# Kernel tuning notes

Hardware: AMD Instinct MI355X
Metric: run time of the kernel (lower is better)

## Reference

```python
import jax, jax.numpy as jnp
import numpy as np
from jax import lax

FEAT_STRIDE = 16
NMS_THRESH = 0.7
N_PRE = 6000   # test-mode n_test_pre_nms
N_POST = 300   # test-mode n_test_post_nms
MIN_SIZE = 16.0
SCALE = 1.0
RATIOS = (0.5, 1.0, 2.0)
ANCHOR_SCALES = (8, 16, 32)
BASE = 16
N_ANCHOR = len(RATIOS) * len(ANCHOR_SCALES)  # 9


def _anchor_base():
    py = px = BASE / 2.0
    ab = np.zeros((N_ANCHOR, 4), np.float32)
    for i, r in enumerate(RATIOS):
        for j, s in enumerate(ANCHOR_SCALES):
            h = BASE * s * np.sqrt(r)
            w = BASE * s * np.sqrt(1.0 / r)
            k = i * len(ANCHOR_SCALES) + j
            ab[k] = [py - h / 2.0, px - w / 2.0, py + h / 2.0, px + w / 2.0]
    return ab


def _anchors(hh, ww):
    # enumerate_shifted_anchor: (y1,x1,y2,x2) anchors for every feature cell
    ab = _anchor_base()
    sy = np.arange(0, hh * FEAT_STRIDE, FEAT_STRIDE)
    sx = np.arange(0, ww * FEAT_STRIDE, FEAT_STRIDE)
    SX, SY = np.meshgrid(sx, sy)
    shift = np.stack([SY.ravel(), SX.ravel(), SY.ravel(), SX.ravel()], 1)
    anc = (ab[None, :, :] + shift[:, None, :]).reshape(-1, 4).astype(np.float32)
    return jnp.asarray(anc)


def _iou(b):
    # b: [N,4] (y1,x1,y2,x2) -> [N,N] IoU
    y1, x1, y2, x2 = b[:, 0], b[:, 1], b[:, 2], b[:, 3]
    area = (y2 - y1) * (x2 - x1)
    ih = jnp.clip(jnp.minimum(y2[:, None], y2[None, :]) - jnp.maximum(y1[:, None], y1[None, :]), 0.0)
    iw = jnp.clip(jnp.minimum(x2[:, None], x2[None, :]) - jnp.maximum(x1[:, None], x1[None, :]), 0.0)
    inter = ih * iw
    return inter / (area[:, None] + area[None, :] - inter + 1e-9)


def _propose(loc, fg, anchor, img_h, img_w):
    # loc:[M,4] fg:[M] anchor:[M,4]  -> padded [N_POST,4] rois + valid mask
    ah = anchor[:, 2] - anchor[:, 0]
    aw = anchor[:, 3] - anchor[:, 1]
    acy = anchor[:, 0] + 0.5 * ah
    acx = anchor[:, 1] + 0.5 * aw
    cy = loc[:, 0] * ah + acy
    cx = loc[:, 1] * aw + acx
    h = jnp.exp(loc[:, 2]) * ah
    w = jnp.exp(loc[:, 3]) * aw
    roi = jnp.stack([
        jnp.clip(cy - 0.5 * h, 0.0, img_h),
        jnp.clip(cx - 0.5 * w, 0.0, img_w),
        jnp.clip(cy + 0.5 * h, 0.0, img_h),
        jnp.clip(cx + 0.5 * w, 0.0, img_w),
    ], axis=1)
    hs = roi[:, 2] - roi[:, 0]
    ws = roi[:, 3] - roi[:, 1]
    ms = MIN_SIZE * SCALE
    valid = (hs >= ms) & (ws >= ms)
    sc = jnp.where(valid, fg, -jnp.inf)  # drop too-small boxes from ranking
    top_sc, idx = lax.top_k(sc, N_PRE)   # score-sorted pre-NMS candidates
    boxes = roi[idx]
    ok = lax.stop_gradient(jnp.isfinite(top_sc))
    sup = lax.stop_gradient(_iou(boxes) > NMS_THRESH)  # [N_PRE,N_PRE]
    tri = jnp.arange(N_PRE)

    def body(i, keep):
        suppressed = jnp.any(keep & sup[:, i] & (tri < i))
        return keep.at[i].set(ok[i] & ~suppressed)

    keep = lax.fori_loop(0, N_PRE, body, jnp.zeros((N_PRE,), bool))
    rank = jnp.cumsum(keep.astype(jnp.int32)) - 1
    sel = keep & (rank < N_POST)
    tgt = jnp.where(sel, rank, N_POST)  # N_POST is out-of-bounds -> dropped
    out = jnp.zeros((N_POST, 4), boxes.dtype).at[tgt].set(boxes, mode='drop')
    vmask = jnp.zeros((N_POST,), bool).at[tgt].set(True, mode='drop')
    return out, vmask


def reference(x, conv1_w, conv1_b, score_w, score_b, loc_w, loc_b, img_h, img_w):
    n, _, hh, ww = x.shape
    anchor = _anchors(hh, ww)
    h = jax.nn.relu(
        lax.conv_general_dilated(x, conv1_w, (1, 1), 'SAME',
                                 dimension_numbers=('NCHW', 'OIHW', 'NCHW'))
        + conv1_b[None, :, None, None])
    locs = jnp.einsum('nchw,oc->nohw', h, loc_w[:, :, 0, 0]) + loc_b[None, :, None, None]
    scr = jnp.einsum('nchw,oc->nohw', h, score_w[:, :, 0, 0]) + score_b[None, :, None, None]
    rpn_locs = locs.transpose(0, 2, 3, 1).reshape(n, -1, 4)          # [n,M,4]
    scr_t = scr.transpose(0, 2, 3, 1)                                 # [n,hh,ww,2A]
    soft = jax.nn.softmax(scr_t.reshape(n, hh, ww, N_ANCHOR, 2), axis=-1)
    fg = soft[..., 1].reshape(n, -1)                                  # [n,M]
    rpn_scores = scr_t.reshape(n, -1, 2)
    rois, vmask = jax.vmap(lambda l, f: _propose(l, f, anchor, img_h, img_w))(rpn_locs, fg)
    roi_indices = jnp.broadcast_to(jnp.arange(n, dtype=jnp.int32)[:, None], (n, N_POST))
    return rpn_locs, rpn_scores, rois, roi_indices, anchor, vmask


def setup_inputs() -> dict:
    key = jax.random.key(0)
    ks = jax.random.split(key, 4)
    x = jax.random.normal(ks[0], (2, 512, 64, 64), jnp.float32)
    conv1_w = 0.01 * jax.random.normal(ks[1], (512, 512, 3, 3), jnp.float32)
    conv1_b = jnp.zeros((512,), jnp.float32)
    score_w = 0.01 * jax.random.normal(ks[2], (N_ANCHOR * 2, 512, 1, 1), jnp.float32)
    score_b = jnp.zeros((N_ANCHOR * 2,), jnp.float32)
    loc_w = 0.01 * jax.random.normal(ks[3], (N_ANCHOR * 4, 512, 1, 1), jnp.float32)
    loc_b = jnp.zeros((N_ANCHOR * 4,), jnp.float32)
    return {"x": x, "conv1_w": conv1_w, "conv1_b": conv1_b,
            "score_w": score_w, "score_b": score_b,
            "loc_w": loc_w, "loc_b": loc_b,
            "img_h": 1024, "img_w": 1024}
```

## Files before the change

### kernel.cpp

```cpp
#include <hip/hip_runtime.h>
#include <hip/hip_bf16.h>
#include <math.h>
#include <cstdint>

typedef unsigned long long u64;
typedef unsigned int u32;
typedef _Float16 half8 __attribute__((ext_vector_type(8)));
typedef float floatx4 __attribute__((ext_vector_type(4)));

#define NANCH 36864
#define SEG 65536
#define N_PRE 6000
#define N_POST 300
#define NW 96
#define NPADC 6144
#define CAP 8192

#define O0 0
#define O1 294912
#define O2 442368
#define O3 444768
#define O4 445368
#define O5 592824

#define WS_XHI   0
#define WS_XLO   2097152
#define WS_WHI   4194304
#define WS_WLO   5373952
#define WS_WSLT  6553600
#define WS_WSLB  6586368
#define WS_H     6586432
#define WS_GUARD 10780736
#define WS_FG    0
#define WS_ROI   73728
#define WS_KEYS  368640
#define WS_SBOX  630784
#define WS_ALIVE 679936
#define WS_CBUF  680320
#define WS_HIST  713088
#define WS_CNT   844160
#define WS_MASK  4194304

#define HSCALE 9.5367431640625e-07f

__device__ __forceinline__ void gl_lds16(const void* g, void* l) {
  __builtin_amdgcn_global_load_lds(
      (const __attribute__((address_space(1))) u32*)g,
      (__attribute__((address_space(3))) u32*)l, 16, 0, 0);
}

__device__ __forceinline__ u64 bcast64(u64 v, int src) {
  u32 lo = (u32)__shfl((int)(v & 0xFFFFFFFFull), src);
  u32 hi = (u32)__shfl((int)(v >> 32), src);
  return ((u64)hi << 32) | lo;
}

__global__ __launch_bounds__(256) void prep_all(
    const float* __restrict__ x, const float* __restrict__ w,
    const float* __restrict__ lw, const float* __restrict__ sw,
    const float* __restrict__ lb, const float* __restrict__ sb,
    float4* __restrict__ h, float4* __restrict__ guard,
    _Float16* __restrict__ xhi, _Float16* __restrict__ xlo,
    _Float16* __restrict__ whi, _Float16* __restrict__ wlo,
    float* __restrict__ wslt, float* __restrict__ wslb) {
  __shared__ float s[64 * 65];
  const int b = blockIdx.x, tid = threadIdx.x;
  if (b < 4097) {
    int idx = b * 256 + tid;
    if (idx < 1048576) h[idx] = make_float4(0.f, 0.f, 0.f, 0.f);
    else if (idx < 1048576 + 16) guard[idx - 1048576] = make_float4(0.f, 0.f, 0.f, 0.f);
    return;
  }
  if (b < 5121) {
    int l = b - 4097;
    int pt = l & 63, cg = (l >> 6) & 7, n = l >> 9;
    const int c0 = cg << 6, p0 = pt << 6;
#pragma unroll
    for (int kk = 0; kk < 16; ++kk) {
      int e = tid + (kk << 8);
      int ci = e >> 6, pi = e & 63;
      s[ci * 65 + pi] = x[(((size_t)(n * 512 + c0 + ci)) << 12) + p0 + pi];
    }
    __syncthreads();
#pragma unroll
    for (int kk = 0; kk < 16; ++kk) {
      int e = tid + (kk << 8);
      int ci = e & 63, pi = e >> 6;
      float sv = s[ci * 65 + pi] * 1024.f;
      _Float16 hi = (_Float16)sv;
      _Float16 lo = (_Float16)(sv - (float)hi);
      size_t off = (((size_t)(n << 12) + p0 + pi) << 9) + c0 + ci;
      xhi[off] = hi;
      xlo[off] = lo;
    }
    return;
  }
  if (b < 5697) {
    int l = b - 5121;
    int ct = l & 7, ot = (l >> 3) & 7, t = l >> 6;
    const int c0 = ct << 6, o0 = ot << 6;
#pragma unroll
    for (int kk = 0; kk < 16; ++kk) {
      int e = tid + (kk << 8);
      int ci = e & 63, oi = e >> 6;
      float sv = w[(size_t)(o0 + oi) * 4608 + (c0 + ci) * 9 + t] * 1024.f;
      _Float16 hi = (_Float16)sv;
      _Float16 lo = (_Float16)(sv - (float)hi);
      size_t off = ((size_t)((t << 9) + o0 + oi) << 9) + c0 + ci;
      whi[off] = hi;
      wlo[off] = lo;
    }
    return;
  }
  {
    int e = (b - 5697) * 256 + tid;
    if (e < 32768) {
      int c = e >> 6, o = e & 63;
      float v = 0.f;
      if (o < 36) v = lw[o * 512 + c];
      else if (o < 54) v = sw[(o - 36) * 512 + c];
      wslt[e] = v;
    } else if (e < 32832) {
      int o = e - 32768;
      float v = 0.f;
      if (o < 36) v = lb[o];
      else if (o < 54) v = sb[o - 36];
      wslb[o] = v;
    }
  }
}

__global__ __launch_bounds__(256) void conv_mfma(
    const _Float16* __restrict__ xhi, const _Float16* __restrict__ xlo,
    const _Float16* __restrict__ whi, const _Float16* __restrict__ wlo,
    const float* __restrict__ guard, float* __restrict__ hout) {
  __shared__ _Float16 aHi[4 * 68 * 32];
  __shared__ _Float16 aLo[4 * 68 * 32];
  __shared__ _Float16 bHi[128 * 32];
  __shared__ _Float16 bLo[128 * 32];
  const int tid = threadIdx.x;
  const int lane = tid & 63, w = tid >> 6;
  const int ptile = blockIdx.x;
  const int og = blockIdx.y;
  const int kq = blockIdx.z;
  const int n = ptile >> 5;
  const int y0 = (ptile & 31) << 1;
  const int o0 = og << 7;
  const int l15 = lane & 15, l16 = lane >> 4;
  const int ry = w >> 1;
  const int wo = (w & 1) << 6;

  floatx4 acc[4][4];
#pragma unroll
  for (int a = 0; a < 4; ++a)
#pragma unroll
    for (int b = 0; b < 4; ++b) acc[a][b] = (floatx4)0.f;

  for (int s = 0; s < 8; ++s) {
    const int c0 = (kq << 8) + (s << 5);
    __syncthreads();
    for (int i = w; i < 17; i += 4) {
      int chunk = (i << 6) + lane;
      int p = chunk >> 2, q = chunk & 3;
      int r = p / 68, xs = p - r * 68;
      int y = y0 - 1 + r, xg = xs - 1;
      bool ok = ((unsigned)y < 64u) && ((unsigned)xg < 64u);
      size_t off = (((size_t)(n << 12) + (y << 6) + xg) << 9) + c0 + (q << 3);
      const void* gh = ok ? (const void*)(xhi + off) : (const void*)guard;
      const void* gl = ok ? (const void*)(xlo + off) : (const void*)guard;
      gl_lds16(gh, (char*)aHi + (i << 10));
      gl_lds16(gl, (char*)aLo + (i << 10));
    }
    for (int tt = 0; tt < 9; ++tt) {
      if (tt > 0) __syncthreads();
      for (int i = w; i < 8; i += 4) {
        int chunk = (i << 6) + lane;
        int row = chunk >> 2, q = chunk & 3;
        size_t off = ((size_t)((tt << 9) + o0 + row) << 9) + c0 + (q << 3);
        gl_lds16((const void*)(whi + off), (char*)bHi + (i << 10));
        gl_lds16((const void*)(wlo + off), (char*)bLo + (i << 10));
      }
      __syncthreads();

      const int dy = tt / 3, dx = tt - 3 * dy;
      half8 ah[4], al[4], bh[4], bl[4];
#pragma unroll
      for (int im = 0; im < 4; ++im) {
        int xp = (im << 4) + l15;
        int p = (ry + dy) * 68 + xp + dx;
        ah[im] = *(const half8*)&aHi[(p << 5) + (l16 << 3)];
        al[im] = *(const half8*)&aLo[(p << 5) + (l16 << 3)];
      }
#pragma unroll
      for (int in = 0; in < 4; ++in) {
        int orow = wo + (in << 4) + l15;
        bh[in] = *(const half8*)&bHi[(orow << 5) + (l16 << 3)];
        bl[in] = *(const half8*)&bLo[(orow << 5) + (l16 << 3)];
      }
#pragma unroll
      for (int im = 0; im < 4; ++im)
#pragma unroll
        for (int in = 0; in < 4; ++in) {
          acc[im][in] = __builtin_amdgcn_mfma_f32_16x16x32_f16(
              ah[im], bh[in], acc[im][in], 0, 0, 0);
          acc[im][in] = __builtin_amdgcn_mfma_f32_16x16x32_f16(
              ah[im], bl[in], acc[im][in], 0, 0, 0);
          acc[im][in] = __builtin_amdgcn_mfma_f32_16x16x32_f16(
              al[im], bh[in], acc[im][in], 0, 0, 0);
        }
    }
  }

#pragma unroll
  for (int im = 0; im < 4; ++im)
#pragma unroll
    for (int in = 0; in < 4; ++in) {
      int o = o0 + wo + (in << 4) + l15;
#pragma unroll
      for (int reg = 0; reg < 4; ++reg) {
        int m_local = (ry << 6) + (im << 4) + (l16 << 2) + reg;
        size_t off = (((size_t)(n << 12) + (y0 << 6) + m_local) << 9) + o;
        atomicAdd(&hout[off], acc[im][in][reg]);
      }
    }
}

__global__ __launch_bounds__(256) void head_kernel(
    const float* __restrict__ hbuf, const float* __restrict__ cb,
    const float* __restrict__ wslt, const float* __restrict__ wslb,
    float* __restrict__ out, float* __restrict__ fgbuf) {
  const int y = blockIdx.x, n = blockIdx.y;
  __shared__ float sH[16 * 65];
  __shared__ float sWt[1024];
  __shared__ float sOut[64 * 65];
  const int tid = threadIdx.x;
  const int x = tid & 63, og = tid >> 6;

  float acc[16];
#pragma unroll
  for (int j = 0; j < 16; ++j) acc[j] = 0.f;

  const float* hb = hbuf + (((size_t)(n << 12) + (y << 6)) << 9);

  for (int c0 = 0; c0 < 512; c0 += 16) {
    __syncthreads();
#pragma unroll
    for (int p = 0; p < 4; ++p) {
      int e = tid + (p << 8);
      {
        int cc = e & 15, xx = e >> 4;
        float raw = hb[((size_t)xx << 9) + c0 + cc];
        sH[cc * 65 + xx] = fmaxf(raw * HSCALE + cb[c0 + cc], 0.f);
      }
      {
        int cc = e >> 6, xx = e & 63;
        sWt[e] = wslt[((c0 + cc) << 6) + xx];
      }
    }
    __syncthreads();
#pragma unroll
    for (int cc = 0; cc < 16; ++cc) {
      float hv = sH[cc * 65 + x];
      const float4* wp = (const float4*)&sWt[(cc << 6) + (og << 4)];
      float4 w0 = wp[0], w1 = wp[1], w2 = wp[2], w3 = wp[3];
      acc[0]  = fmaf(hv, w0.x, acc[0]);  acc[1]  = fmaf(hv, w0.y, acc[1]);
      acc[2]  = fmaf(hv, w0.z, acc[2]);  acc[3]  = fmaf(hv, w0.w, acc[3]);
      acc[4]  = fmaf(hv, w1.x, acc[4]);  acc[5]  = fmaf(hv, w1.y, acc[5]);
      acc[6]  = fmaf(hv, w1.z, acc[6]);  acc[7]  = fmaf(hv, w1.w, acc[7]);
      acc[8]  = fmaf(hv, w2.x, acc[8]);  acc[9]  = fmaf(hv, w2.y, acc[9]);
      acc[10] = fmaf(hv, w2.z, acc[10]); acc[11] = fmaf(hv, w2.w, acc[11]);
      acc[12] = fmaf(hv, w3.x, acc[12]); acc[13] = fmaf(hv, w3.y, acc[13]);
      acc[14] = fmaf(hv, w3.z, acc[14]); acc[15] = fmaf(hv, w3.w, acc[15]);
    }
  }
  __syncthreads();
#pragma unroll
  for (int j = 0; j < 16; ++j) {
    int o = (og << 4) + j;
    sOut[o * 65 + x] = acc[j] + wslb[o];
  }
  __syncthreads();

  const int p0 = (n << 12) + (y << 6);
  float* locs = out + O0 + (size_t)p0 * 36;
  for (int e = tid; e < 2304; e += 256) {
    int xx = e / 36, o = e - xx * 36;
    locs[e] = sOut[o * 65 + xx];
  }
  float* scrs = out + O1 + (size_t)p0 * 18;
  for (int e = tid; e < 1152; e += 256) {
    int xx = e / 18, ss = e - xx * 18;
    scrs[e] = sOut[(36 + ss) * 65 + xx];
  }
  float* fg = fgbuf + n * NANCH + (y << 6) * 9;
  for (int e = tid; e < 576; e += 256) {
    int xx = e / 9, a = e - xx * 9;
    float s0 = sOut[(36 + 2 * a) * 65 + xx];
    float s1 = sOut[(36 + 2 * a + 1) * 65 + xx];
    fg[e] = 1.0f / (1.0f + expf(s0 - s1));
  }
}

__global__ __launch_bounds__(256) void decode_kernel(
    const float* __restrict__ out0, const float* __restrict__ fgbuf,
    float4* __restrict__ roibuf, u64* __restrict__ keys,
    float* __restrict__ anchor_out, float* __restrict__ out,
    u32* __restrict__ hist, u64* __restrict__ cbuf, u32* __restrict__ cnt,
    const int* __restrict__ imgh_p, const int* __restrict__ imgw_p) {
  int gid = blockIdx.x * 256 + threadIdx.x;
  hist[gid] = 0u;
  if (gid < 2 * CAP) cbuf[gid] = ~0ull;
  if (gid < 4) cnt[gid] = 0u;
  if (gid < 3600) {
    if (gid < 2400) out[O2 + gid] = 0.f;
    else if (gid < 3000) out[O3 + (gid - 2400)] = (float)((gid - 2400) / 300);
    else out[O5 + (gid - 3000)] = 0.f;
  }
  int n = gid >> 16, k = gid & (SEG - 1);
  if (k >= NANCH) return;
  int a = k % 9;
  int p = k / 9;
  int py = p >> 6, px = p & 63;

  const double R[3] = {0.5, 1.0, 2.0};
  const double S[3] = {8.0, 16.0, 32.0};
  double r = R[a / 3], s = S[a - (a / 3) * 3];
  double hd = 16.0 * s * sqrt(r);
  double wd = 16.0 * s * sqrt(1.0 / r);
  float ay1 = (float)(8.0 - hd / 2.0) + (float)(py * 16);
  float ax1 = (float)(8.0 - wd / 2.0) + (float)(px * 16);
  float ay2 = (float)(8.0 + hd / 2.0) + (float)(py * 16);
  float ax2 = (float)(8.0 + wd / 2.0) + (float)(px * 16);
  if (n == 0) {
    float* ao = anchor_out + (size_t)k * 4;
    ao[0] = ay1; ao[1] = ax1; ao[2] = ay2; ao[3] = ax2;
  }
  float ahk = ay2 - ay1, awk = ax2 - ax1;
  float acy = ay1 + 0.5f * ahk, acx = ax1 + 0.5f * awk;
  const float* lp = out0 + ((size_t)(n * NANCH + k) << 2);
  float dy = lp[0], dx = lp[1], dh = lp[2], dw = lp[3];
  float cy = dy * ahk + acy;
  float cx = dx * awk + acx;
  float bh = expf(dh) * ahk;
  float bw = expf(dw) * awk;
  float img_h = (float)imgh_p[0], img_w = (float)imgw_p[0];
  float y1 = fminf(fmaxf(cy - 0.5f * bh, 0.f), img_h);
  float x1 = fminf(fmaxf(cx - 0.5f * bw, 0.f), img_w);
  float y2 = fminf(fmaxf(cy + 0.5f * bh, 0.f), img_h);
  float x2 = fminf(fmaxf(cx + 0.5f * bw, 0.f), img_w);
  bool valid = ((y2 - y1) >= 16.f) && ((x2 - x1) >= 16.f);
  float sc = valid ? fgbuf[n * NANCH + k] : -INFINITY;
  roibuf[n * NANCH + k] = make_float4(y1, x1, y2, x2);
  unsigned int b = __float_as_uint(sc);
  unsigned int m = b ^ ((b & 0x80000000u) ? 0xFFFFFFFFu : 0x80000000u);
  keys[gid] = ((u64)(~m) << 32) | (unsigned int)k;
}

__global__ __launch_bounds__(256) void hist_kernel(
    const u64* __restrict__ keys, u32* __restrict__ hist) {
  const int n = blockIdx.y;
  int i = blockIdx.x * 256 + threadIdx.x;
  u32 hk = (u32)(keys[(n << 16) + i] >> 32);
  if (hk < 0xFF800000u) atomicAdd(&hist[(n << 16) + (hk >> 16)], 1u);
}

__global__ __launch_bounds__(1024) void thresh_kernel(
    const u32* __restrict__ hist, u32* __restrict__ cnt) {
  const int n = blockIdx.x, t = threadIdx.x;
  __shared__ u32 sc[1024];
  const uint4* hp = (const uint4*)(hist + (n << 16));
  u32 s = 0;
#pragma unroll
  for (int q = 0; q < 16; ++q) {
    uint4 v = hp[t * 16 + q];
    s += v.x + v.y + v.z + v.w;
  }
  sc[t] = s;
  __syncthreads();
  for (int off = 1; off < 1024; off <<= 1) {
    u32 v = (t >= off) ? sc[t - off] : 0u;
    __syncthreads();
    sc[t] += v;
    __syncthreads();
  }
  u32 total = sc[1023];
  u32 target = total < (u32)N_PRE ? total : (u32)N_PRE;
  u32 mycum = sc[t];
  u32 prev = t ? sc[t - 1] : 0u;
  if (total > 0 && mycum >= target && prev < target) {
    u32 base = prev;
    int b = t << 6;
    while (true) {
      base += hist[(n << 16) + b];
      if (base >= target) break;
      ++b;
    }
    cnt[2 + n] = (u32)b;
  }
}

__global__ __launch_bounds__(256) void compact_kernel(
    const u64* __restrict__ keys, u32* __restrict__ cnt,
    u64* __restrict__ cbuf) {
  const int n = blockIdx.y;
  int i = blockIdx.x * 256 + threadIdx.x;
  u64 key = keys[(n << 16) + i];
  u32 hk = (u32)(key >> 32);
  u32 T = cnt[2 + n];
  if (hk < 0xFF800000u && (hk >> 16) <= T) {
    u32 slot = atomicAdd(&cnt[n], 1u);
    if (slot < (u32)CAP) cbuf[(n << 13) + slot] = key;
  }
}

__global__ __launch_bounds__(1024) void sortgather_kernel(
    const u64* __restrict__ cbuf, const float4* __restrict__ roibuf,
    float4* __restrict__ sbox, u64* __restrict__ alive) {
  __shared__ u64 sk[CAP];
  const int n = blockIdx.x, t = threadIdx.x;
  for (int e = t; e < CAP; e += 1024) sk[e] = cbuf[(n << 13) + e];
  __syncthreads();
  for (int k = 2; k <= CAP; k <<= 1) {
    for (int j = k >> 1; j > 0; j >>= 1) {
      for (int q = t; q < (CAP >> 1); q += 1024) {
        int l = ((q & ~(j - 1)) << 1) | (q & (j - 1));
        int rr = l | j;
        bool asc = ((l & k) == 0);
        u64 a = sk[l], b = sk[rr];
        if ((a > b) == asc) { sk[l] = b; sk[rr] = a; }
      }
      __syncthreads();
    }
  }
  for (int i = t; i < NPADC; i += 1024) {
    u64 kk = sk[i];
    bool valid = (i < N_PRE) && ((u32)(kk >> 32) < 0xFF800000u);
    float4 b = make_float4(0.f, 0.f, 0.f, 0.f);
    if (valid) b = roibuf[(size_t)n * NANCH + (u32)(kk & 0xFFFFFFFFull)];
    sbox[n * NPADC + i] = b;
    u64 bal = __ballot(valid);
    if ((t & 63) == 0) alive[n * NW + (i >> 6)] = bal;
  }
}

__global__ __launch_bounds__(256) void build_mask(
    const float4* __restrict__ sbox, u64* __restrict__ M) {
  __shared__ float4 jb[4][64];
  __shared__ float ja[4][64];
  const int tid = threadIdx.x, lane = tid & 63, wv = tid >> 6;
  const int g = blockIdx.x, q = blockIdx.y, n = blockIdx.z;
  const float4* sb = sbox + n * NPADC;
  float4 bi = sb[(g << 6) + lane];
  float ai = (bi.z - bi.x) * (bi.w - bi.y);
  u64* Mrow = M + ((size_t)(n * NPADC + (g << 6) + lane)) * NW;
#pragma unroll
  for (int it = 0; it < 6; ++it) {
    int w = q * 24 + (it << 2) + wv;
    float4 bjl = sb[(w << 6) + lane];
    jb[wv][lane] = bjl;
    ja[wv][lane] = (bjl.z - bjl.x) * (bjl.w - bjl.y);
    u64 bits = 0;
#pragma unroll 8
    for (int j = 0; j < 64; ++j) {
      float4 bj = jb[wv][j];
      float aj = ja[wv][j];
      float ih = fmaxf(fminf(bi.z, bj.z) - fmaxf(bi.x, bj.x), 0.f);
      float iw = fmaxf(fminf(bi.w, bj.w) - fmaxf(bi.y, bj.y), 0.f);
      float inter = ih * iw;
      bool bit = inter / (ai + aj - inter + 1e-9f) > 0.7f;
      bits |= ((u64)bit) << j;
    }
    Mrow[w] = bits;
  }
}

__global__ __launch_bounds__(64) void nms_reduce(
    const u64* __restrict__ M, const u64* __restrict__ alive,
    const float4* __restrict__ sbox, float* __restrict__ out) {
  const int n = blockIdx.x, lane = threadIdx.x;
  float* rois = out + O2 + n * (N_POST * 4);
  float* vmask = out + O5 + n * N_POST;
  const u64* A = alive + n * NW;
  const u64* Mb = M + (size_t)n * NPADC * NW;
  const float4* sb = sbox + n * NPADC;
  u64 aw0 = A[lane];
  u64 aw1 = (lane < 32) ? A[64 + lane] : 0ull;
  u64 accA = 0, accB = 0;
  int nk = 0;
  u64 dnext = Mb[(size_t)lane * NW + 0];
  float4 bnext = sb[lane];
  const u64 below = lane ? (~0ull >> (64 - lane)) : 0ull;

  for (int c = 0; c < 94; ++c) {
    u64 dcur = dnext;
    float4 bcur = bnext;
    if (c + 1 < 94) {
      dnext = Mb[(size_t)(((c + 1) << 6) + lane) * NW + (c + 1)];
      bnext = sb[((c + 1) << 6) + lane];
    }
    u64 wacc = (c < 64) ? bcast64(accA, c) : bcast64(accB, c - 64);
    u64 aw = (c < 64) ? bcast64(aw0, c) : bcast64(aw1, c - 64);
    u64 alive_u = aw & ~wacc;
    if (alive_u == 0ull) continue;

    u64 dmask = dcur & below;
    u64 rem = alive_u, kept = 0;
    while (rem) {
      int j = __builtin_ctzll(rem);
      kept |= 1ull << j;
      u64 col = __ballot((dmask >> j) & 1);
      rem &= ~(col | (1ull << j));
    }

    int npop = __popcll(kept);
    if ((kept >> lane) & 1ull) {
      int slot = nk + __popcll(kept & below);
      if (slot < N_POST) {
        rois[slot * 4 + 0] = bcur.x; rois[slot * 4 + 1] = bcur.y;
        rois[slot * 4 + 2] = bcur.z; rois[slot * 4 + 3] = bcur.w;
        vmask[slot] = 1.0f;
      }
    }
    if (nk + npop >= N_POST) break;
    nk += npop;

    u64 kk = kept;
    while (kk) {
      int j0 = __builtin_ctzll(kk); kk &= kk - 1;
      int j1 = kk ? __builtin_ctzll(kk) : j0; kk &= kk - 1;
      int j2 = kk ? __builtin_ctzll(kk) : j0; kk &= kk - 1;
      int j3 = kk ? __builtin_ctzll(kk) : j0; kk &= kk - 1;
      int j4 = kk ? __builtin_ctzll(kk) : j0; kk &= kk - 1;
      int j5 = kk ? __builtin_ctzll(kk) : j0; kk &= kk - 1;
      int j6 = kk ? __builtin_ctzll(kk) : j0; kk &= kk - 1;
      int j7 = kk ? __builtin_ctzll(kk) : j0; kk &= kk - 1;
      const u64* r0 = Mb + (size_t)((c << 6) + j0) * NW;
      const u64* r1 = Mb + (size_t)((c << 6) + j1) * NW;
      const u64* r2 = Mb + (size_t)((c << 6) + j2) * NW;
      const u64* r3 = Mb + (size_t)((c << 6) + j3) * NW;
      const u64* r4 = Mb + (size_t)((c << 6) + j4) * NW;
      const u64* r5 = Mb + (size_t)((c << 6) + j5) * NW;
      const u64* r6 = Mb + (size_t)((c << 6) + j6) * NW;
      const u64* r7 = Mb + (size_t)((c << 6) + j7) * NW;
      u64 oA = r0[lane] | r1[lane] | r2[lane] | r3[lane]
             | r4[lane] | r5[lane] | r6[lane] | r7[lane];
      u64 oB = 0;
      if (lane < 32)
        oB = r0[64 + lane] | r1[64 + lane] | r2[64 + lane] | r3[64 + lane]
           | r4[64 + lane] | r5[64 + lane] | r6[64 + lane] | r7[64 + lane];
      accA |= oA;
      accB |= oB;
    }
  }
}

extern "C" void kernel_launch(void* const* d_in, const int* in_sizes, int n_in,
                              void* d_out, int out_size, void* d_ws, size_t ws_size,
                              hipStream_t stream) {
  const float* x        = (const float*)d_in[0];
  const float* conv1_w  = (const float*)d_in[1];
  const float* conv1_b  = (const float*)d_in[2];
  const float* score_w  = (const float*)d_in[3];
  const float* score_b  = (const float*)d_in[4];
  const float* loc_w    = (const float*)d_in[5];
  const float* loc_b    = (const float*)d_in[6];
  const int*   imgh_p   = (const int*)d_in[7];
  const int*   imgw_p   = (const int*)d_in[8];

  float* out = (float*)d_out;
  float* ws  = (float*)d_ws;

  _Float16* xhi = (_Float16*)(ws + WS_XHI);
  _Float16* xlo = (_Float16*)(ws + WS_XLO);
  _Float16* whi = (_Float16*)(ws + WS_WHI);
  _Float16* wlo = (_Float16*)(ws + WS_WLO);
  float* wslt   = ws + WS_WSLT;
  float* wslb   = ws + WS_WSLB;
  float* hbuf   = ws + WS_H;
  float* guard  = ws + WS_GUARD;
  float* fgbuf   = ws + WS_FG;
  float4* roibuf = (float4*)(ws + WS_ROI);
  u64* keys      = (u64*)(ws + WS_KEYS);
  float4* sbox   = (float4*)(ws + WS_SBOX);
  u64* alive     = (u64*)(ws + WS_ALIVE);
  u64* cbuf      = (u64*)(ws + WS_CBUF);
  u32* hist      = (u32*)(ws + WS_HIST);
  u32* cnt       = (u32*)(ws + WS_CNT);
  u64* maskbuf   = (u64*)(ws + WS_MASK);

  prep_all<<<5826, 256, 0, stream>>>(x, conv1_w, loc_w, score_w, loc_b, score_b,
                                     (float4*)hbuf, (float4*)guard,
                                     xhi, xlo, whi, wlo, wslt, wslb);

  conv_mfma<<<dim3(64, 4, 2), 256, 0, stream>>>(xhi, xlo, whi, wlo, guard, hbuf);

  head_kernel<<<dim3(64, 2), 256, 0, stream>>>(hbuf, conv1_b, wslt, wslb, out, fgbuf);
  decode_kernel<<<512, 256, 0, stream>>>(out, fgbuf, roibuf, keys,
                                         out + O4, out, hist, cbuf, cnt,
                                         imgh_p, imgw_p);

  hist_kernel<<<dim3(144, 2), 256, 0, stream>>>(keys, hist);
  thresh_kernel<<<2, 1024, 0, stream>>>(hist, cnt);
  compact_kernel<<<dim3(144, 2), 256, 0, stream>>>(keys, cnt, cbuf);
  sortgather_kernel<<<2, 1024, 0, stream>>>(cbuf, roibuf, sbox, alive);

  build_mask<<<dim3(96, 4, 2), 256, 0, stream>>>(sbox, maskbuf);
  nms_reduce<<<2, 64, 0, stream>>>(maskbuf, alive, sbox, out);
}
```

Baseline: 500.1 us.

## Fuse histogram, threshold, compaction and sort into fewer kernels

```diff
diff --git a/kernel.cpp b/kernel.cpp
--- a/kernel.cpp
+++ b/kernel.cpp
@@ -38,7 +38,6 @@
 #define WS_ALIVE 679936
 #define WS_CBUF  680320
 #define WS_HIST  713088
-#define WS_CNT   844160
 #define WS_MASK  4194304
 
 #define HSCALE 9.5367431640625e-07f
@@ -228,13 +227,19 @@
 __global__ __launch_bounds__(256) void head_kernel(
     const float* __restrict__ hbuf, const float* __restrict__ cb,
     const float* __restrict__ wslt, const float* __restrict__ wslb,
-    float* __restrict__ out, float* __restrict__ fgbuf) {
+    float* __restrict__ out, float* __restrict__ fgbuf,
+    uint4* __restrict__ hist4) {
   const int y = blockIdx.x, n = blockIdx.y;
   __shared__ float sH[16 * 65];
   __shared__ float sWt[1024];
   __shared__ float sOut[64 * 65];
   const int tid = threadIdx.x;
   const int x = tid & 63, og = tid >> 6;
+
+  {
+    int gid = ((n << 6) + y) * 256 + tid;
+    hist4[gid] = make_uint4(0u, 0u, 0u, 0u);
+  }
 
   float acc[16];
 #pragma unroll
@@ -305,12 +310,9 @@
     const float* __restrict__ out0, const float* __restrict__ fgbuf,
     float4* __restrict__ roibuf, u64* __restrict__ keys,
     float* __restrict__ anchor_out, float* __restrict__ out,
-    u32* __restrict__ hist, u64* __restrict__ cbuf, u32* __restrict__ cnt,
+    u32* __restrict__ hist,
     const int* __restrict__ imgh_p, const int* __restrict__ imgw_p) {
   int gid = blockIdx.x * 256 + threadIdx.x;
-  hist[gid] = 0u;
-  if (gid < 2 * CAP) cbuf[gid] = ~0ull;
-  if (gid < 4) cnt[gid] = 0u;
   if (gid < 3600) {
     if (gid < 2400) out[O2 + gid] = 0.f;
     else if (gid < 3000) out[O3 + (gid - 2400)] = (float)((gid - 2400) / 300);
@@ -353,21 +355,20 @@
   roibuf[n * NANCH + k] = make_float4(y1, x1, y2, x2);
   unsigned int b = __float_as_uint(sc);
   unsigned int m = b ^ ((b & 0x80000000u) ? 0xFFFFFFFFu : 0x80000000u);
-  keys[gid] = ((u64)(~m) << 32) | (unsigned int)k;
-}
-
-__global__ __launch_bounds__(256) void hist_kernel(
-    const u64* __restrict__ keys, u32* __restrict__ hist) {
-  const int n = blockIdx.y;
-  int i = blockIdx.x * 256 + threadIdx.x;
-  u32 hk = (u32)(keys[(n << 16) + i] >> 32);
+  u32 hk = ~m;
+  keys[gid] = ((u64)hk << 32) | (unsigned int)k;
   if (hk < 0xFF800000u) atomicAdd(&hist[(n << 16) + (hk >> 16)], 1u);
 }
 
-__global__ __launch_bounds__(1024) void thresh_kernel(
-    const u32* __restrict__ hist, u32* __restrict__ cnt) {
+__global__ __launch_bounds__(1024) void select_kernel(
+    const u32* __restrict__ hist, const u64* __restrict__ keys,
+    const float4* __restrict__ roibuf,
+    float4* __restrict__ sbox, u64* __restrict__ alive) {
+  __shared__ u64 sk[CAP];
+  __shared__ u32 sT, sCnt;
+  u32* sc = (u32*)sk;
   const int n = blockIdx.x, t = threadIdx.x;
-  __shared__ u32 sc[1024];
+
   const uint4* hp = (const uint4*)(hist + (n << 16));
   u32 s = 0;
 #pragma unroll
@@ -375,6 +376,7 @@
     uint4 v = hp[t * 16 + q];
     s += v.x + v.y + v.z + v.w;
   }
+  if (t == 0) { sT = 0u; sCnt = 0u; }
   sc[t] = s;
   __syncthreads();
   for (int off = 1; off < 1024; off <<= 1) {
@@ -387,6 +389,7 @@
   u32 target = total < (u32)N_PRE ? total : (u32)N_PRE;
   u32 mycum = sc[t];
   u32 prev = t ? sc[t - 1] : 0u;
+  __syncthreads();
   if (total > 0 && mycum >= target && prev < target) {
     u32 base = prev;
     int b = t << 6;
@@ -395,31 +398,24 @@
       if (base >= target) break;
       ++b;
     }
-    cnt[2 + n] = (u32)b;
-  }
-}
-
-__global__ __launch_bounds__(256) void compact_kernel(
-    const u64* __restrict__ keys, u32* __restrict__ cnt,
-    u64* __restrict__ cbuf) {
-  const int n = blockIdx.y;
-  int i = blockIdx.x * 256 + threadIdx.x;
-  u64 key = keys[(n << 16) + i];
-  u32 hk = (u32)(key >> 32);
-  u32 T = cnt[2 + n];
-  if (hk < 0xFF800000u && (hk >> 16) <= T) {
-    u32 slot = atomicAdd(&cnt[n], 1u);
-    if (slot < (u32)CAP) cbuf[(n << 13) + slot] = key;
-  }
-}
-
-__global__ __launch_bounds__(1024) void sortgather_kernel(
-    const u64* __restrict__ cbuf, const float4* __restrict__ roibuf,
-    float4* __restrict__ sbox, u64* __restrict__ alive) {
-  __shared__ u64 sk[CAP];
-  const int n = blockIdx.x, t = threadIdx.x;
-  for (int e = t; e < CAP; e += 1024) sk[e] = cbuf[(n << 13) + e];
+    sT = (u32)b;
+  }
   __syncthreads();
+  const u32 T = sT;
+  const bool any = (total > 0);
+
+  for (int e = t; e < CAP; e += 1024) sk[e] = ~0ull;
+  __syncthreads();
+  for (int i = t; i < NANCH; i += 1024) {
+    u64 key = keys[(n << 16) + i];
+    u32 hk = (u32)(key >> 32);
+    if (any && hk < 0xFF800000u && (hk >> 16) <= T) {
+      u32 slot = atomicAdd(&sCnt, 1u);
+      if (slot < (u32)CAP) sk[slot] = key;
+    }
+  }
+  __syncthreads();
+
   for (int k = 2; k <= CAP; k <<= 1) {
     for (int j = k >> 1; j > 0; j >>= 1) {
       for (int q = t; q < (CAP >> 1); q += 1024) {
@@ -432,6 +428,7 @@
       __syncthreads();
     }
   }
+
   for (int i = t; i < NPADC; i += 1024) {
     u64 kk = sk[i];
     bool valid = (i < N_PRE) && ((u32)(kk >> 32) < 0xFF800000u);
@@ -583,9 +580,7 @@
   u64* keys      = (u64*)(ws + WS_KEYS);
   float4* sbox   = (float4*)(ws + WS_SBOX);
   u64* alive     = (u64*)(ws + WS_ALIVE);
-  u64* cbuf      = (u64*)(ws + WS_CBUF);
   u32* hist      = (u32*)(ws + WS_HIST);
-  u32* cnt       = (u32*)(ws + WS_CNT);
   u64* maskbuf   = (u64*)(ws + WS_MASK);
 
   prep_all<<<5826, 256, 0, stream>>>(x, conv1_w, loc_w, score_w, loc_b, score_b,
@@ -594,15 +589,12 @@
 
   conv_mfma<<<dim3(64, 4, 2), 256, 0, stream>>>(xhi, xlo, whi, wlo, guard, hbuf);
 
-  head_kernel<<<dim3(64, 2), 256, 0, stream>>>(hbuf, conv1_b, wslt, wslb, out, fgbuf);
+  head_kernel<<<dim3(64, 2), 256, 0, stream>>>(hbuf, conv1_b, wslt, wslb, out,
+                                               fgbuf, (uint4*)hist);
   decode_kernel<<<512, 256, 0, stream>>>(out, fgbuf, roibuf, keys,
-                                         out + O4, out, hist, cbuf, cnt,
-                                         imgh_p, imgw_p);
-
-  hist_kernel<<<dim3(144, 2), 256, 0, stream>>>(keys, hist);
-  thresh_kernel<<<2, 1024, 0, stream>>>(hist, cnt);
-  compact_kernel<<<dim3(144, 2), 256, 0, stream>>>(keys, cnt, cbuf);
-  sortgather_kernel<<<2, 1024, 0, stream>>>(cbuf, roibuf, sbox, alive);
+                                         out + O4, out, hist, imgh_p, imgw_p);
+
+  select_kernel<<<2, 1024, 0, stream>>>(hist, keys, roibuf, sbox, alive);
 
   build_mask<<<dim3(96, 4, 2), 256, 0, stream>>>(sbox, maskbuf);
   nms_reduce<<<2, 64, 0, stream>>>(maskbuf, alive, sbox, out);
```

Result: no change. 495.3 us (-1.0%).
